# Optimization experiments

Measured on AMD Instinct MI355X. Metric: run time of the kernel, lower is better.

## Reference

```python
import jax, jax.numpy as jnp
import numpy as np

D_MODEL = 2048
NUM_Q_HEADS = 32
NUM_KV_HEADS = 8
HEAD_DIM = D_MODEL // NUM_Q_HEADS  # 64
NUM_GROUPS = NUM_Q_HEADS // NUM_KV_HEADS  # 4


def setup_inputs() -> dict:
    key = jax.random.key(0)
    ks = jax.random.split(key, 9)
    s = 1.0 / np.sqrt(D_MODEL)
    x = jax.random.normal(ks[0], (2, 2048, D_MODEL), dtype=jnp.float32)
    Wq = jax.random.uniform(ks[1], (D_MODEL, NUM_Q_HEADS * HEAD_DIM), jnp.float32, -s, s)
    bq = jax.random.uniform(ks[2], (NUM_Q_HEADS * HEAD_DIM,), jnp.float32, -s, s)
    Wk = jax.random.uniform(ks[3], (D_MODEL, NUM_KV_HEADS * HEAD_DIM), jnp.float32, -s, s)
    bk = jax.random.uniform(ks[4], (NUM_KV_HEADS * HEAD_DIM,), jnp.float32, -s, s)
    Wv = jax.random.uniform(ks[5], (D_MODEL, NUM_KV_HEADS * HEAD_DIM), jnp.float32, -s, s)
    bv = jax.random.uniform(ks[6], (NUM_KV_HEADS * HEAD_DIM,), jnp.float32, -s, s)
    Wo = jax.random.uniform(ks[7], (D_MODEL, D_MODEL), jnp.float32, -s, s)
    bo = jax.random.uniform(ks[8], (D_MODEL,), jnp.float32, -s, s)
    return {"x": x, "Wq": Wq, "bq": bq, "Wk": Wk, "bk": bk,
            "Wv": Wv, "bv": bv, "Wo": Wo, "bo": bo}


def reference(x, Wq, bq, Wk, bk, Wv, bv, Wo, bo):
    B, T, C = x.shape
    Hkv, G, Dh = NUM_KV_HEADS, NUM_GROUPS, HEAD_DIM
    # projections
    q = (x @ Wq + bq).reshape(B, T, Hkv, G, Dh)   # group G query heads per kv head
    k = (x @ Wk + bk).reshape(B, T, Hkv, Dh)
    v = (x @ Wv + bv).reshape(B, T, Hkv, Dh)
    scale = 1.0 / np.sqrt(Dh).astype(np.float32)
    # scores: [B, Hkv, G, T, T] (kv head broadcast over its G query heads)
    scores = jnp.einsum('btkgd,bskd->bkgts', q, k) * scale
    attn = jax.nn.softmax(scores, axis=-1)
    out = jnp.einsum('bkgts,bskd->btkgd', attn, v).reshape(B, T, C)
    return out @ Wo + bo
```

## Files before the change

kernel.cpp:

```cpp
#include <hip/hip_runtime.h>
#include <cstdint>
#include <cstddef>
#include <math.h>

typedef uint16_t bf16;
typedef __attribute__((ext_vector_type(8))) __bf16 bf16x8;
typedef __attribute__((ext_vector_type(2))) float f32x2;
typedef __attribute__((ext_vector_type(4))) float f32x4;
typedef __attribute__((ext_vector_type(16))) float f32x16;

#define MFMA16(a,b,c) __builtin_amdgcn_mfma_f32_16x16x32_bf16((a),(b),(c),0,0,0)
#define MFMA32(a,b,c) __builtin_amdgcn_mfma_f32_32x32x16_bf16((a),(b),(c),0,0,0)

__device__ __forceinline__ uint16_t f2bf(float f){
  uint32_t u = __float_as_uint(f);
  return (uint16_t)((u + 0x7fffu + ((u >> 16) & 1u)) >> 16);
}
__device__ __forceinline__ uint32_t pk2(float lo, float hi){
  return (uint32_t)f2bf(lo) | ((uint32_t)f2bf(hi) << 16);
}

__device__ __forceinline__ void gload_lds16(const void* g, void* l){
  __builtin_amdgcn_global_load_lds((const __attribute__((address_space(1))) void*)g,
                                   (__attribute__((address_space(3))) void*)l, 16, 0, 0);
}

__global__ void k_convert(const float* __restrict__ in, bf16* __restrict__ out, int n){
  int i = (blockIdx.x * 256 + threadIdx.x) * 4;
  if (i >= n) return;
  float4 v = *reinterpret_cast<const float4*>(in + i);
  uint32_t lo = pk2(v.x, v.y);
  uint32_t hi = pk2(v.z, v.w);
  uint2 pkv = make_uint2(lo, hi);
  *reinterpret_cast<uint2*>(out + i) = pkv;
}

__global__ void k_transposeW(const float* __restrict__ in, bf16* __restrict__ out, int R, int C){
  __shared__ float tile[64][65];
  int c0 = blockIdx.x * 64, r0 = blockIdx.y * 64;
  int t = threadIdx.x;
  int fx = t & 15, fy = t >> 4;
  #pragma unroll
  for (int i = 0; i < 4; i++){
    int r = fy + i*16;
    float4 v = *reinterpret_cast<const float4*>(in + (size_t)(r0 + r)*C + c0 + fx*4);
    tile[r][fx*4+0] = v.x; tile[r][fx*4+1] = v.y;
    tile[r][fx*4+2] = v.z; tile[r][fx*4+3] = v.w;
  }
  __syncthreads();
  int gx = t & 7, gy = t >> 3;
  #pragma unroll
  for (int i = 0; i < 2; i++){
    int c = gy + i*32;
    int rr = gx*8;
    union { bf16 h[8]; uint4 u; } pk_;
    #pragma unroll
    for (int j = 0; j < 8; j++) pk_.h[j] = f2bf(tile[rr+j][c]);
    *reinterpret_cast<uint4*>(out + (size_t)(c0 + c)*R + r0 + rr) = pk_.u;
  }
}

__device__ __forceinline__ void gemm256_core(
    const bf16* __restrict__ Abase, const bf16* __restrict__ Btbase,
    char* lds, f32x4 acc[8][4])
{
  const int tid = threadIdx.x;
  const int wid = tid >> 6, lane = tid & 63;
  const int wm = wid >> 2, wn = wid & 3;
  const int lr = lane & 15, lg = lane >> 4;
  const f32x4 vzero = {0.f, 0.f, 0.f, 0.f};
  #pragma unroll
  for (int m = 0; m < 8; m++)
    #pragma unroll
    for (int n = 0; n < 4; n++)
      acc[m][n] = vzero;

  int srcH[2];
  #pragma unroll
  for (int i = 0; i < 2; i++){
    int db = i*8192 + tid*16;
    int row = db >> 7, sp = (db >> 4) & 7, sl = sp ^ (row & 7);
    srcH[i] = row*2048 + sl*8;
  }
  const int dOf = wid*1024;

  int ksl[2];
  #pragma unroll
  for (int ks = 0; ks < 2; ks++) ksl[ks] = (((ks*4 + lg) ^ (lr & 7)) << 4);
  const int aB = wm*16384 + lr*128;
  const int bB = 32768 + (wn >> 1)*16384 + (wn & 1)*8192 + lr*128;

  const bf16* Ab1 = Abase + 128*2048;
  const bf16* Bb1 = Btbase + 128*2048;

  #define STG_HALF(dstOff, gsrc) do { \
    gload_lds16((gsrc) + srcH[0], lds + (dstOff) + dOf); \
    gload_lds16((gsrc) + srcH[1], lds + (dstOff) + 8192 + dOf); \
  } while(0)

  STG_HALF(0,     Abase);
  STG_HALF(16384, Ab1);
  STG_HALF(32768, Btbase);
  STG_HALF(49152, Bb1);
  STG_HALF(65536, Abase + 64);
  asm volatile("s_waitcnt vmcnt(2)" ::: "memory");
  __builtin_amdgcn_s_barrier();

  bf16x8 afr[4][2], bfr[4][2];
  for (int t = 0; t < 32; t++){
    const int bo = (t & 1) * 65536;
    const int nb = bo ^ 65536;

    #pragma unroll
    for (int am = 0; am < 4; am++)
      #pragma unroll
      for (int ks = 0; ks < 2; ks++)
        afr[am][ks] = *reinterpret_cast<const bf16x8*>(lds + bo + aB + am*2048 + ksl[ks]);
    #pragma unroll
    for (int bn = 0; bn < 2; bn++)
      #pragma unroll
      for (int ks = 0; ks < 2; ks++)
        bfr[bn][ks] = *reinterpret_cast<const bf16x8*>(lds + bo + bB + bn*2048 + ksl[ks]);
    if (t < 31) STG_HALF(nb + 16384, Ab1 + (t+1)*64);
    __builtin_amdgcn_s_barrier();
    asm volatile("s_waitcnt lgkmcnt(0)" ::: "memory");
    __builtin_amdgcn_sched_barrier(0);
    __builtin_amdgcn_s_setprio(1);
    #pragma unroll
    for (int am = 0; am < 4; am++)
      #pragma unroll
      for (int bn = 0; bn < 2; bn++)
        #pragma unroll
        for (int ks = 0; ks < 2; ks++)
          acc[am][bn] = MFMA16(afr[am][ks], bfr[bn][ks], acc[am][bn]);
    __builtin_amdgcn_s_setprio(0);
    __builtin_amdgcn_s_barrier();

    #pragma unroll
    for (int bn = 2; bn < 4; bn++)
      #pragma unroll
      for (int ks = 0; ks < 2; ks++)
        bfr[bn][ks] = *reinterpret_cast<const bf16x8*>(lds + bo + bB + bn*2048 + ksl[ks]);
    if (t < 31) STG_HALF(nb + 32768, Btbase + (t+1)*64);
    __builtin_amdgcn_s_barrier();
    asm volatile("s_waitcnt lgkmcnt(0)" ::: "memory");
    __builtin_amdgcn_sched_barrier(0);
    __builtin_amdgcn_s_setprio(1);
    #pragma unroll
    for (int am = 0; am < 4; am++)
      #pragma unroll
      for (int bn = 2; bn < 4; bn++)
        #pragma unroll
        for (int ks = 0; ks < 2; ks++)
          acc[am][bn] = MFMA16(afr[am][ks], bfr[bn][ks], acc[am][bn]);
    __builtin_amdgcn_s_setprio(0);
    __builtin_amdgcn_s_barrier();

    #pragma unroll
    for (int am = 0; am < 4; am++)
      #pragma unroll
      for (int ks = 0; ks < 2; ks++)
        afr[am][ks] = *reinterpret_cast<const bf16x8*>(lds + bo + aB + (am+4)*2048 + ksl[ks]);
    if (t < 31) STG_HALF(nb + 49152, Bb1 + (t+1)*64);
    __builtin_amdgcn_s_barrier();
    asm volatile("s_waitcnt lgkmcnt(0)" ::: "memory");
    __builtin_amdgcn_sched_barrier(0);
    __builtin_amdgcn_s_setprio(1);
    #pragma unroll
    for (int am = 0; am < 4; am++)
      #pragma unroll
      for (int bn = 0; bn < 2; bn++)
        #pragma unroll
        for (int ks = 0; ks < 2; ks++)
          acc[am+4][bn] = MFMA16(afr[am][ks], bfr[bn][ks], acc[am+4][bn]);
    __builtin_amdgcn_s_setprio(0);
    __builtin_amdgcn_s_barrier();

    if (t < 30) STG_HALF(bo, Abase + (t+2)*64);
    __builtin_amdgcn_s_barrier();
    __builtin_amdgcn_s_setprio(1);
    #pragma unroll
    for (int am = 0; am < 4; am++)
      #pragma unroll
      for (int bn = 2; bn < 4; bn++)
        #pragma unroll
        for (int ks = 0; ks < 2; ks++)
          acc[am+4][bn] = MFMA16(afr[am][ks], bfr[bn][ks], acc[am+4][bn]);
    __builtin_amdgcn_s_setprio(0);
    if (t < 30)      asm volatile("s_waitcnt vmcnt(2)" ::: "memory");
    else if (t == 30) asm volatile("s_waitcnt vmcnt(0)" ::: "memory");
    __builtin_amdgcn_sched_barrier(0);
    __builtin_amdgcn_s_barrier();
  }
  #undef STG_HALF
}

__device__ __forceinline__ void gemm256x128_core(
    const bf16* __restrict__ Abase, const bf16* __restrict__ Btbase,
    char* lds, f32x4 acc[2][8])
{
  const int tid = threadIdx.x;
  const int wid = tid >> 6, lane = tid & 63;
  const int lr = lane & 15, lg = lane >> 4;
  const f32x4 vzero = {0.f, 0.f, 0.f, 0.f};
  #pragma unroll
  for (int m = 0; m < 2; m++)
    #pragma unroll
    for (int n = 0; n < 8; n++)
      acc[m][n] = vzero;

  int srcH[2];
  #pragma unroll
  for (int i = 0; i < 2; i++){
    int db = i*8192 + tid*16;
    int row = db >> 7, sp = (db >> 4) & 7, sl = sp ^ (row & 7);
    srcH[i] = row*2048 + sl*8;
  }
  const int dOf = wid*1024;

  int ksl[2];
  #pragma unroll
  for (int ks = 0; ks < 2; ks++) ksl[ks] = (((ks*4 + lg) ^ (lr & 7)) << 4);
  const int aB = wid*4096 + lr*128;
  const int bB = lr*128;

  const bf16* Ab1 = Abase + 128*2048;

  #define STG16(dstOff, gsrc) do { \
    gload_lds16((gsrc) + srcH[0], lds + (dstOff) + dOf); \
    gload_lds16((gsrc) + srcH[1], lds + (dstOff) + 8192 + dOf); \
  } while(0)
  #define STG_A(bufOff, koff) do { \
    STG16((bufOff),         Abase + (koff)); \
    STG16((bufOff) + 16384, Ab1  + (koff)); \
  } while(0)

  STG_A(0, 0);
  STG16(98304, Btbase);
  STG_A(32768, 64);
  asm volatile("s_waitcnt vmcnt(4)" ::: "memory");
  __builtin_amdgcn_s_barrier();

  int aOff = 0;
  int aStg = 65536;
  bf16x8 afr[2], bfr[8];
  for (int t = 0; t < 32; t++){
    const int bOff = 98304 + (t & 1) * 16384;
    const int nbOff = bOff ^ 16384;

    #pragma unroll
    for (int am = 0; am < 2; am++)
      afr[am] = *reinterpret_cast<const bf16x8*>(lds + aOff + aB + am*2048 + ksl[0]);
    #pragma unroll
    for (int bn = 0; bn < 8; bn++)
      bfr[bn] = *reinterpret_cast<const bf16x8*>(lds + bOff + bB + bn*2048 + ksl[0]);
    if (t < 31) STG16(nbOff, Btbase + (t+1)*64);
    __builtin_amdgcn_s_barrier();
    asm volatile("s_waitcnt lgkmcnt(0)" ::: "memory");
    __builtin_amdgcn_sched_barrier(0);
    __builtin_amdgcn_s_setprio(1);
    #pragma unroll
    for (int am = 0; am < 2; am++)
      #pragma unroll
      for (int bn = 0; bn < 8; bn++)
        acc[am][bn] = MFMA16(afr[am], bfr[bn], acc[am][bn]);
    __builtin_amdgcn_s_setprio(0);
    __builtin_amdgcn_s_barrier();

    #pragma unroll
    for (int am = 0; am < 2; am++)
      afr[am] = *reinterpret_cast<const bf16x8*>(lds + aOff + aB + am*2048 + ksl[1]);
    #pragma unroll
    for (int bn = 0; bn < 8; bn++)
      bfr[bn] = *reinterpret_cast<const bf16x8*>(lds + bOff + bB + bn*2048 + ksl[1]);
    if (t < 30) STG_A(aStg, (t+2)*64);
    __builtin_amdgcn_s_barrier();
    asm volatile("s_waitcnt lgkmcnt(0)" ::: "memory");
    __builtin_amdgcn_sched_barrier(0);
    __builtin_amdgcn_s_setprio(1);
    #pragma unroll
    for (int am = 0; am < 2; am++)
      #pragma unroll
      for (int bn = 0; bn < 8; bn++)
        acc[am][bn] = MFMA16(afr[am], bfr[bn], acc[am][bn]);
    __builtin_amdgcn_s_setprio(0);
    if (t < 30)       asm volatile("s_waitcnt vmcnt(4)" ::: "memory");
    else if (t == 30) asm volatile("s_waitcnt vmcnt(0)" ::: "memory");
    __builtin_amdgcn_sched_barrier(0);
    __builtin_amdgcn_s_barrier();

    aOff = (aOff == 65536) ? 0 : aOff + 32768;
    aStg = (aStg == 65536) ? 0 : aStg + 32768;
  }
  #undef STG16
  #undef STG_A
}

__global__ __launch_bounds__(512, 1) void k_qkv(
    const bf16* __restrict__ xb,
    const bf16* __restrict__ WqT, const bf16* __restrict__ WkT, const bf16* __restrict__ WvT,
    const float* __restrict__ bq, const float* __restrict__ bk, const float* __restrict__ bv,
    bf16* __restrict__ qo, bf16* __restrict__ ko, bf16* __restrict__ vtp)
{
  __shared__ __align__(16) char lds[131072];
  int by = blockIdx.y;
  const bf16* Bt; const float* bias; int mode; int y; float scale = 1.f;
  if (by < 8){       y = by;    Bt = WqT + (size_t)y*256*2048; bias = bq + y*256; mode = 0; scale = 0.18033688011112042f; }
  else if (by < 10){ y = by-8;  Bt = WkT + (size_t)y*256*2048; bias = bk + y*256; mode = 1; }
  else {             y = by-10; Bt = WvT + (size_t)y*256*2048; bias = bv + y*256; mode = 2; }
  int m0 = blockIdx.x * 256;
  f32x4 acc[8][4];
  gemm256_core(xb + (size_t)m0*2048, Bt, lds, acc);
  const int tid = threadIdx.x, wid = tid >> 6, lane = tid & 63;
  const int wm = wid >> 2, wn = wid & 3, lr = lane & 15, lg = lane >> 4;
  if (mode == 2){
    #pragma unroll
    for (int bn = 0; bn < 4; bn++){
      int c = wn*64 + bn*16 + lr;
      float bb = bias[c];
      int CL = y*256 + c;
      #pragma unroll
      for (int am = 0; am < 8; am++){
        int row0 = m0 + wm*128 + am*16 + lg*4;
        int bi = row0 >> 11, tl = row0 & 2047;
        union { bf16 h[4]; uint2 u; } pk_;
        #pragma unroll
        for (int r = 0; r < 4; r++) pk_.h[r] = f2bf(acc[am][bn][r] + bb);
        *reinterpret_cast<uint2*>(vtp + ((size_t)bi*512 + CL)*2048 + tl) = pk_.u;
      }
    }
  } else {
    bf16* outp = (mode == 0) ? (qo + y*256) : (ko + y*256);
    int ldc = (mode == 0) ? 2048 : 512;
    #pragma unroll
    for (int bn = 0; bn < 4; bn++){
      int c = wn*64 + bn*16 + lr;
      float bb = bias[c];
      #pragma unroll
      for (int am = 0; am < 8; am++)
        #pragma unroll
        for (int r = 0; r < 4; r++){
          int row = m0 + wm*128 + am*16 + lg*4 + r;
          outp[(size_t)row*ldc + c] = f2bf((acc[am][bn][r] + bb) * scale);
        }
    }
  }
}

__global__ __launch_bounds__(512, 1) void k_oproj(
    const bf16* __restrict__ ab, const bf16* __restrict__ WoT,
    const float* __restrict__ bo, float* __restrict__ outp)
{
  __shared__ __align__(16) char lds[131072];
  int m0 = blockIdx.x * 256, n0 = blockIdx.y * 128;
  f32x4 acc[2][8];
  gemm256x128_core(ab + (size_t)m0*2048, WoT + (size_t)n0*2048, lds, acc);
  const int tid = threadIdx.x, wid = tid >> 6, lane = tid & 63;
  const int lr = lane & 15, lg = lane >> 4;
  #pragma unroll
  for (int bn = 0; bn < 8; bn++){
    int col = n0 + bn*16 + lr;
    float bb = bo[col];
    #pragma unroll
    for (int am = 0; am < 2; am++)
      #pragma unroll
      for (int r = 0; r < 4; r++){
        int row = m0 + wid*32 + am*16 + lg*4 + r;
        outp[(size_t)row*2048 + col] = acc[am][bn][r] + bb;
      }
  }
}

__global__ __launch_bounds__(512, 2) void k_flash(
    const bf16* __restrict__ q, const bf16* __restrict__ kmat,
    const bf16* __restrict__ vt, bf16* __restrict__ ao)
{
  __shared__ __align__(16) char lds[98304];
  const int tid = threadIdx.x;
  const int wid = tid >> 6, lane = tid & 63;
  const int l31 = lane & 31, hi = lane >> 5;
  const int bh = blockIdx.y;
  const int b = bh >> 5, hq = bh & 31, kvh = hq >> 2;
  const int qt = blockIdx.x;
  const int qrow0 = b*2048 + qt*512 + wid*64;

  bf16x8 qf[2][4];
  #pragma unroll
  for (int g = 0; g < 2; g++){
    const bf16* qrow = q + (size_t)(qrow0 + g*32 + l31)*2048 + hq*64 + hi*8;
    #pragma unroll
    for (int t = 0; t < 4; t++)
      qf[g][t] = *reinterpret_cast<const bf16x8*>(qrow + t*16);
  }

  f32x16 oacc[2][2];
  #pragma unroll
  for (int g = 0; g < 2; g++)
    #pragma unroll
    for (int n = 0; n < 2; n++)
      #pragma unroll
      for (int r = 0; r < 16; r++) oacc[g][n][r] = 0.f;
  float rsg[2][2];
  rsg[0][0]=0.f; rsg[0][1]=0.f; rsg[1][0]=0.f; rsg[1][1]=0.f;
  const f32x16 zv = {0.f,0.f,0.f,0.f,0.f,0.f,0.f,0.f,0.f,0.f,0.f,0.f,0.f,0.f,0.f,0.f};

  const int r7 = l31 & 7;
  int A[4];
  #pragma unroll
  for (int j = 0; j < 4; j++)
    A[j] = l31*128 + (((2*j + hi) ^ r7) << 4);

  const bf16* kbase = kmat + (size_t)b*2048*512 + kvh*64;
  const bf16* vbase = vt + ((size_t)b*512 + kvh*64)*2048;

  int kSrc[2], vSrc[2];
  const int dOf = wid*1024;
  #pragma unroll
  for (int i = 0; i < 2; i++){
    int kdb = i*8192 + tid*16;
    int krow = kdb >> 7, ksp = (kdb >> 4) & 7, ksl = ksp ^ (krow & 7);
    kSrc[i] = krow*512 + ksl*8;
    int o = tid*16;
    int vrow = o >> 7, vsp = (o >> 4) & 7, vsl = vsp ^ (vrow & 7);
    vSrc[i] = vrow*2048 + i*64 + vsl*8;
  }

  #define STAGE(bo, st_) do { \
    const bf16* kb_ = kbase + (size_t)(st_)*128*512; \
    const bf16* vb_ = vbase + (st_)*128; \
    gload_lds16(kb_ + kSrc[0], lds + (bo) + dOf); \
    gload_lds16(kb_ + kSrc[1], lds + (bo) + 8192 + dOf); \
    gload_lds16(vb_ + vSrc[0], lds + 49152 + (bo) + dOf); \
    gload_lds16(vb_ + vSrc[1], lds + 49152 + (bo) + 8192 + dOf); \
  } while(0)

  #define LDK(j, imm) (*reinterpret_cast<const bf16x8*>(lds + kOff + A[j] + (imm)))
  #define LDV(j, imm) (*reinterpret_cast<const bf16x8*>(lds + 49152 + kOff + A[j] + (imm)))

  STAGE(0, 0);
  STAGE(16384, 1);

  int kOff = 0;
  int sOff = 32768;
  for (int st = 0; st < 16; st++){
    if (st == 15) asm volatile("s_waitcnt vmcnt(0)" ::: "memory");
    else          asm volatile("s_waitcnt vmcnt(4)" ::: "memory");
    __builtin_amdgcn_sched_barrier(0);
    __builtin_amdgcn_s_barrier();
    __builtin_amdgcn_sched_barrier(0);
    if (st < 14){
      STAGE(sOff, st+2);
      sOff = (sOff == 32768) ? 0 : sOff + 16384;
    }

    #pragma unroll
    for (int c = 0; c < 2; c++){
      f32x16 sc[2][2];
      __builtin_amdgcn_s_setprio(1);
      #pragma unroll
      for (int t = 0; t < 4; t++){
        bf16x8 af0 = LDK(t, c*8192);
        bf16x8 af1 = LDK(t, c*8192 + 4096);
        if (t == 0){
          sc[0][0] = MFMA32(af0, qf[0][0], zv);
          sc[1][0] = MFMA32(af0, qf[1][0], zv);
          sc[0][1] = MFMA32(af1, qf[0][0], zv);
          sc[1][1] = MFMA32(af1, qf[1][0], zv);
        } else {
          sc[0][0] = MFMA32(af0, qf[0][t], sc[0][0]);
          sc[1][0] = MFMA32(af0, qf[1][t], sc[1][0]);
          sc[0][1] = MFMA32(af1, qf[0][t], sc[0][1]);
          sc[1][1] = MFMA32(af1, qf[1][t], sc[1][1]);
        }
      }
      __builtin_amdgcn_s_setprio(0);

      uint32_t pw[2][2][8];
      #pragma unroll
      for (int g = 0; g < 2; g++){
        #pragma unroll
        for (int n = 0; n < 2; n++)
          #pragma unroll
          for (int j = 0; j < 8; j++){
            float plo = __builtin_amdgcn_exp2f(sc[g][n][2*j]);
            float phi = __builtin_amdgcn_exp2f(sc[g][n][2*j+1]);
            rsg[g][j & 1] += plo + phi;
            asm("v_cvt_pk_bf16_f32 %0, %1, %2" : "=v"(pw[g][n][j]) : "v"(plo), "v"(phi));
          }
        #pragma unroll
        for (int n = 0; n < 2; n++)
          #pragma unroll
          for (int h = 0; h < 2; h++){
            asm volatile("v_permlane32_swap_b32 %0, %1" : "+v"(pw[g][n][h*4+0]), "+v"(pw[g][n][h*4+2]));
            asm volatile("v_permlane32_swap_b32 %0, %1" : "+v"(pw[g][n][h*4+1]), "+v"(pw[g][n][h*4+3]));
          }
      }

      __builtin_amdgcn_s_setprio(1);
      #pragma unroll
      for (int kk = 0; kk < 4; kk++){
        int n = kk >> 1, h = kk & 1;
        union { uint32_t w[4]; bf16x8 v; } pa0, pa1;
        #pragma unroll
        for (int w_ = 0; w_ < 4; w_++){ pa0.w[w_] = pw[0][n][h*4+w_]; pa1.w[w_] = pw[1][n][h*4+w_]; }
        #pragma unroll
        for (int nd = 0; nd < 2; nd++){
          bf16x8 vf = LDV(kk, c*8192 + nd*4096);
          oacc[0][nd] = MFMA32(pa0.v, vf, oacc[0][nd]);
          oacc[1][nd] = MFMA32(pa1.v, vf, oacc[1][nd]);
        }
      }
      __builtin_amdgcn_s_setprio(0);
    }
    kOff = (kOff == 32768) ? 0 : kOff + 16384;
  }
  #undef STAGE
  #undef LDK
  #undef LDV

  #pragma unroll
  for (int g = 0; g < 2; g++){
    float rs = rsg[g][0] + rsg[g][1];
    float l = rs + __shfl_xor(rs, 32);
    float linv = 1.f / l;
    float lv[16];
    #pragma unroll
    for (int r = 0; r < 16; r++){
      int qi = (r & 3) + 8*(r >> 2) + 4*hi;
      lv[r] = __shfl(linv, qi);
    }
    #pragma unroll
    for (int nd = 0; nd < 2; nd++)
      #pragma unroll
      for (int r = 0; r < 16; r++){
        int qi = (r & 3) + 8*(r >> 2) + 4*hi;
        int row = qrow0 + g*32 + qi;
        ao[(size_t)row*2048 + hq*64 + nd*32 + l31] = f2bf(oacc[g][nd][r] * lv[r]);
      }
  }
}

extern "C" void kernel_launch(void* const* d_in, const int* in_sizes, int n_in,
                              void* d_out, int out_size, void* d_ws, size_t ws_size,
                              hipStream_t stream)
{
  const float* x  = (const float*)d_in[0];
  const float* Wq = (const float*)d_in[1];
  const float* bq = (const float*)d_in[2];
  const float* Wk = (const float*)d_in[3];
  const float* bk = (const float*)d_in[4];
  const float* Wv = (const float*)d_in[5];
  const float* bv = (const float*)d_in[6];
  const float* Wo = (const float*)d_in[7];
  const float* bo = (const float*)d_in[8];
  float* out = (float*)d_out;

  char* ws = (char*)d_ws;
  size_t off = 0;
  auto alloc = [&](size_t bytes){ char* p = ws + off; off += (bytes + 255) & ~(size_t)255; return p; };
  bf16* xb  = (bf16*)alloc(2*2048*2048*2);
  bf16* WqT = (bf16*)alloc(2048*2048*2);
  bf16* WkT = (bf16*)alloc(512*2048*2);
  bf16* WvT = (bf16*)alloc(512*2048*2);
  bf16* WoT = (bf16*)alloc(2048*2048*2);
  bf16* qb  = (bf16*)alloc(4096*2048*2);
  bf16* kb  = (bf16*)alloc((size_t)4096*512*2);
  bf16* vtb = (bf16*)alloc((size_t)4096*512*2);
  bf16* aob = xb;

  k_convert<<<8192, 256, 0, stream>>>(x, xb, 2*2048*2048);
  k_transposeW<<<dim3(32,32), 256, 0, stream>>>(Wq, WqT, 2048, 2048);
  k_transposeW<<<dim3(8,32),  256, 0, stream>>>(Wk, WkT, 2048, 512);
  k_transposeW<<<dim3(8,32),  256, 0, stream>>>(Wv, WvT, 2048, 512);
  k_transposeW<<<dim3(32,32), 256, 0, stream>>>(Wo, WoT, 2048, 2048);
  k_qkv<<<dim3(16,12), 512, 0, stream>>>(xb, WqT, WkT, WvT, bq, bk, bv, qb, kb, vtb);
  k_flash<<<dim3(4,64), 512, 0, stream>>>(qb, kb, vtb, aob);
  k_oproj<<<dim3(16,16), 512, 0, stream>>>(aob, WoT, bo, out);
}
```

Baseline: 194.4 us.

## Re-tile O-projection warps 2x4 and fuse Wo transpose into QKV launch

The 256x128 O-projection GEMM changes its warp layout from 8x1 (each warp 32 rows by 128 cols) to 2x4 (each warp 128 rows by 32 cols), so each warp reads more A fragments and fewer B fragments from LDS. Separately, the Wo transpose/convert moves out of its own launch and into extra blocks of the QKV kernel (grid y 12 to 16), so it runs alongside the QKV GEMM on otherwise idle CUs and one kernel launch disappears. The fused transpose blocks use the large LDS allocation and 512 threads with single occupancy, which may crowd CU slots during the QKV GEMM.

```diff
diff --git a/kernel.cpp b/kernel.cpp
--- a/kernel.cpp
+++ b/kernel.cpp
@@ -197,81 +197,88 @@
 
 __device__ __forceinline__ void gemm256x128_core(
     const bf16* __restrict__ Abase, const bf16* __restrict__ Btbase,
-    char* lds, f32x4 acc[2][8])
+    char* lds, f32x4 acc[8][2])
 {
   const int tid = threadIdx.x;
   const int wid = tid >> 6, lane = tid & 63;
+  const int wm = wid >> 2, wn = wid & 3;
   const int lr = lane & 15, lg = lane >> 4;
   const f32x4 vzero = {0.f, 0.f, 0.f, 0.f};
   #pragma unroll
-  for (int m = 0; m < 2; m++)
-    #pragma unroll
-    for (int n = 0; n < 8; n++)
+  for (int m = 0; m < 8; m++)
+    #pragma unroll
+    for (int n = 0; n < 2; n++)
       acc[m][n] = vzero;
 
-  int srcH[2];
+  int srcA[4], srcB[2];
+  #pragma unroll
+  for (int i = 0; i < 4; i++){
+    int db = i*8192 + tid*16;
+    int row = db >> 7, sp = (db >> 4) & 7, sl = sp ^ (row & 7);
+    srcA[i] = row*2048 + sl*8;
+  }
   #pragma unroll
   for (int i = 0; i < 2; i++){
     int db = i*8192 + tid*16;
     int row = db >> 7, sp = (db >> 4) & 7, sl = sp ^ (row & 7);
-    srcH[i] = row*2048 + sl*8;
+    srcB[i] = row*2048 + sl*8;
   }
   const int dOf = wid*1024;
 
   int ksl[2];
   #pragma unroll
   for (int ks = 0; ks < 2; ks++) ksl[ks] = (((ks*4 + lg) ^ (lr & 7)) << 4);
-  const int aB = wid*4096 + lr*128;
-  const int bB = lr*128;
-
-  const bf16* Ab1 = Abase + 128*2048;
-
-  #define STG16(dstOff, gsrc) do { \
-    gload_lds16((gsrc) + srcH[0], lds + (dstOff) + dOf); \
-    gload_lds16((gsrc) + srcH[1], lds + (dstOff) + 8192 + dOf); \
+  const int aB = wm*16384 + lr*128;
+  const int bB = wn*4096 + lr*128;
+
+  #define STG_A(bufOff, koff) do { \
+    gload_lds16(Abase + (koff) + srcA[0], lds + (bufOff) + dOf); \
+    gload_lds16(Abase + (koff) + srcA[1], lds + (bufOff) + 8192 + dOf); \
+    gload_lds16(Abase + (koff) + srcA[2], lds + (bufOff) + 16384 + dOf); \
+    gload_lds16(Abase + (koff) + srcA[3], lds + (bufOff) + 24576 + dOf); \
   } while(0)
-  #define STG_A(bufOff, koff) do { \
-    STG16((bufOff),         Abase + (koff)); \
-    STG16((bufOff) + 16384, Ab1  + (koff)); \
+  #define STG_B(bufOff, koff) do { \
+    gload_lds16(Btbase + (koff) + srcB[0], lds + (bufOff) + dOf); \
+    gload_lds16(Btbase + (koff) + srcB[1], lds + (bufOff) + 8192 + dOf); \
   } while(0)
 
   STG_A(0, 0);
-  STG16(98304, Btbase);
+  STG_B(98304, 0);
   STG_A(32768, 64);
   asm volatile("s_waitcnt vmcnt(4)" ::: "memory");
   __builtin_amdgcn_s_barrier();
 
+  bf16x8 afr[8], bfr[2];
   int aOff = 0;
-  int aStg = 65536;
-  bf16x8 afr[2], bfr[8];
   for (int t = 0; t < 32; t++){
-    const int bOff = 98304 + (t & 1) * 16384;
-    const int nbOff = bOff ^ 16384;
-
-    #pragma unroll
-    for (int am = 0; am < 2; am++)
+    const int bOff = 98304 + (t & 1)*16384;
+    const int aNxt2 = (aOff == 65536) ? 0 : aOff + 32768;
+    const int aStg = (aOff == 0) ? 65536 : aOff - 32768;
+
+    #pragma unroll
+    for (int am = 0; am < 8; am++)
       afr[am] = *reinterpret_cast<const bf16x8*>(lds + aOff + aB + am*2048 + ksl[0]);
     #pragma unroll
-    for (int bn = 0; bn < 8; bn++)
+    for (int bn = 0; bn < 2; bn++)
       bfr[bn] = *reinterpret_cast<const bf16x8*>(lds + bOff + bB + bn*2048 + ksl[0]);
-    if (t < 31) STG16(nbOff, Btbase + (t+1)*64);
+    if (t < 31) STG_B(bOff ^ 16384, (t+1)*64);
     __builtin_amdgcn_s_barrier();
     asm volatile("s_waitcnt lgkmcnt(0)" ::: "memory");
     __builtin_amdgcn_sched_barrier(0);
     __builtin_amdgcn_s_setprio(1);
     #pragma unroll
-    for (int am = 0; am < 2; am++)
-      #pragma unroll
-      for (int bn = 0; bn < 8; bn++)
+    for (int am = 0; am < 8; am++)
+      #pragma unroll
+      for (int bn = 0; bn < 2; bn++)
         acc[am][bn] = MFMA16(afr[am], bfr[bn], acc[am][bn]);
     __builtin_amdgcn_s_setprio(0);
     __builtin_amdgcn_s_barrier();
 
     #pragma unroll
-    for (int am = 0; am < 2; am++)
+    for (int am = 0; am < 8; am++)
       afr[am] = *reinterpret_cast<const bf16x8*>(lds + aOff + aB + am*2048 + ksl[1]);
     #pragma unroll
-    for (int bn = 0; bn < 8; bn++)
+    for (int bn = 0; bn < 2; bn++)
       bfr[bn] = *reinterpret_cast<const bf16x8*>(lds + bOff + bB + bn*2048 + ksl[1]);
     if (t < 30) STG_A(aStg, (t+2)*64);
     __builtin_amdgcn_s_barrier();
@@ -279,9 +286,9 @@
     __builtin_amdgcn_sched_barrier(0);
     __builtin_amdgcn_s_setprio(1);
     #pragma unroll
-    for (int am = 0; am < 2; am++)
-      #pragma unroll
-      for (int bn = 0; bn < 8; bn++)
+    for (int am = 0; am < 8; am++)
+      #pragma unroll
+      for (int bn = 0; bn < 2; bn++)
         acc[am][bn] = MFMA16(afr[am], bfr[bn], acc[am][bn]);
     __builtin_amdgcn_s_setprio(0);
     if (t < 30)       asm volatile("s_waitcnt vmcnt(4)" ::: "memory");
@@ -290,20 +297,53 @@
     __builtin_amdgcn_s_barrier();
 
     aOff = (aOff == 65536) ? 0 : aOff + 32768;
-    aStg = (aStg == 65536) ? 0 : aStg + 32768;
-  }
-  #undef STG16
+    (void)aNxt2;
+  }
   #undef STG_A
+  #undef STG_B
 }
 
 __global__ __launch_bounds__(512, 1) void k_qkv(
     const bf16* __restrict__ xb,
     const bf16* __restrict__ WqT, const bf16* __restrict__ WkT, const bf16* __restrict__ WvT,
     const float* __restrict__ bq, const float* __restrict__ bk, const float* __restrict__ bv,
-    bf16* __restrict__ qo, bf16* __restrict__ ko, bf16* __restrict__ vtp)
+    bf16* __restrict__ qo, bf16* __restrict__ ko, bf16* __restrict__ vtp,
+    const float* __restrict__ Wo, bf16* __restrict__ WoT)
 {
   __shared__ __align__(16) char lds[131072];
   int by = blockIdx.y;
+  if (by >= 12){
+    const int tb = (by - 12)*16 + blockIdx.x;
+    const int half = threadIdx.x >> 8;
+    const int t256 = threadIdx.x & 255;
+    float (*tile)[65] = reinterpret_cast<float(*)[65]>(lds + half*16640);
+    #pragma unroll 1
+    for (int p = 0; p < 8; p++){
+      int tIdx = tb*16 + p*2 + half;
+      int c0 = (tIdx & 31)*64, r0 = (tIdx >> 5)*64;
+      int fx = t256 & 15, fy = t256 >> 4;
+      #pragma unroll
+      for (int i = 0; i < 4; i++){
+        int r = fy + i*16;
+        float4 v = *reinterpret_cast<const float4*>(Wo + (size_t)(r0 + r)*2048 + c0 + fx*4);
+        tile[r][fx*4+0] = v.x; tile[r][fx*4+1] = v.y;
+        tile[r][fx*4+2] = v.z; tile[r][fx*4+3] = v.w;
+      }
+      __syncthreads();
+      int gx = t256 & 7, gy = t256 >> 3;
+      #pragma unroll
+      for (int i = 0; i < 2; i++){
+        int c = gy + i*32;
+        int rr = gx*8;
+        union { bf16 h[8]; uint4 u; } pk_;
+        #pragma unroll
+        for (int j = 0; j < 8; j++) pk_.h[j] = f2bf(tile[rr+j][c]);
+        *reinterpret_cast<uint4*>(WoT + (size_t)(c0 + c)*2048 + r0 + rr) = pk_.u;
+      }
+      __syncthreads();
+    }
+    return;
+  }
   const bf16* Bt; const float* bias; int mode; int y; float scale = 1.f;
   if (by < 8){       y = by;    Bt = WqT + (size_t)y*256*2048; bias = bq + y*256; mode = 0; scale = 0.18033688011112042f; }
   else if (by < 10){ y = by-8;  Bt = WkT + (size_t)y*256*2048; bias = bk + y*256; mode = 1; }
@@ -353,19 +393,19 @@
 {
   __shared__ __align__(16) char lds[131072];
   int m0 = blockIdx.x * 256, n0 = blockIdx.y * 128;
-  f32x4 acc[2][8];
+  f32x4 acc[8][2];
   gemm256x128_core(ab + (size_t)m0*2048, WoT + (size_t)n0*2048, lds, acc);
   const int tid = threadIdx.x, wid = tid >> 6, lane = tid & 63;
-  const int lr = lane & 15, lg = lane >> 4;
-  #pragma unroll
-  for (int bn = 0; bn < 8; bn++){
-    int col = n0 + bn*16 + lr;
+  const int wm = wid >> 2, wn = wid & 3, lr = lane & 15, lg = lane >> 4;
+  #pragma unroll
+  for (int bn = 0; bn < 2; bn++){
+    int col = n0 + wn*32 + bn*16 + lr;
     float bb = bo[col];
     #pragma unroll
-    for (int am = 0; am < 2; am++)
+    for (int am = 0; am < 8; am++)
       #pragma unroll
       for (int r = 0; r < 4; r++){
-        int row = m0 + wid*32 + am*16 + lg*4 + r;
+        int row = m0 + wm*128 + am*16 + lg*4 + r;
         outp[(size_t)row*2048 + col] = acc[am][bn][r] + bb;
       }
   }
@@ -572,8 +612,7 @@
   k_transposeW<<<dim3(32,32), 256, 0, stream>>>(Wq, WqT, 2048, 2048);
   k_transposeW<<<dim3(8,32),  256, 0, stream>>>(Wk, WkT, 2048, 512);
   k_transposeW<<<dim3(8,32),  256, 0, stream>>>(Wv, WvT, 2048, 512);
-  k_transposeW<<<dim3(32,32), 256, 0, stream>>>(Wo, WoT, 2048, 2048);
-  k_qkv<<<dim3(16,12), 512, 0, stream>>>(xb, WqT, WkT, WvT, bq, bk, bv, qb, kb, vtb);
+  k_qkv<<<dim3(16,16), 512, 0, stream>>>(xb, WqT, WkT, WvT, bq, bk, bv, qb, kb, vtb, Wo, WoT);
   k_flash<<<dim3(4,64), 512, 0, stream>>>(qb, kb, vtb, aob);
   k_oproj<<<dim3(16,16), 512, 0, stream>>>(aob, WoT, bo, out);
 }
```

Measured after the change: 190.0 us. -2.2%, faster.
